# Kernel optimization log

Hardware: AMD Instinct MI355X
Metric: run time of the kernel (lower is better)

Reference implementation:

```python
import jax, jax.numpy as jnp
import numpy as np

N_NODES = 50000
N_EDGES = 600000
D = 128
EPS = 1e-5
AVG_D_LOG = float(np.log(4 + 1))  # avg_d={'log': log(avg_d+1)}, avg_d=4


def setup_inputs() -> dict:
    key = jax.random.key(0)
    ks = jax.random.split(key, 8)
    h = jax.random.normal(ks[0], (N_NODES, D), dtype=jnp.float32)
    # guarantee every node has at least one incoming edge (self-loop)
    edge_dst = jnp.concatenate([
        jnp.arange(N_NODES, dtype=jnp.int64),
        jax.random.randint(ks[1], (N_EDGES - N_NODES,), 0, N_NODES).astype(jnp.int64),
    ])
    edge_src = jax.random.randint(ks[2], (N_EDGES,), 0, N_NODES).astype(jnp.int64)
    def lin(k, fan_in, fan_out):
        lim = 1.0 / np.sqrt(fan_in)
        return jax.random.uniform(k, (fan_in, fan_out), jnp.float32, -lim, lim)
    W_pre = lin(ks[3], 2 * D, D)
    b_pre = jnp.zeros((D,), jnp.float32)
    W_post = lin(ks[4], 12 * D + D, D)  # 4 aggregators * 3 scalers * D + in_dim
    b_post = jnp.zeros((D,), jnp.float32)
    W_mix = lin(ks[5], D, D)
    b_mix = jnp.zeros((D,), jnp.float32)
    return {"h": h, "edge_src": edge_src, "edge_dst": edge_dst,
            "W_pre": W_pre, "b_pre": b_pre, "W_post": W_post,
            "b_post": b_post, "W_mix": W_mix, "b_mix": b_mix}


def reference(h, edge_src, edge_dst, W_pre, b_pre, W_post, b_post, W_mix, b_mix):
    n = h.shape[0]
    # pretrans_edges: cat(src, dst) -> Linear -> ReLU (MLP act) -> ReLU (outer)
    z2 = jnp.concatenate([h[edge_src], h[edge_dst]], axis=1)        # [E, 2D]
    e = jax.nn.relu(z2 @ W_pre + b_pre)                             # [E, D]
    # multi-aggregator segment reduce over destination nodes
    deg = jax.ops.segment_sum(jnp.ones_like(edge_dst, jnp.float32), edge_dst, n)  # [N]
    inv_deg = 1.0 / deg[:, None]
    mean = jax.ops.segment_sum(e, edge_dst, n) * inv_deg
    mean_sq = jax.ops.segment_sum(e * e, edge_dst, n) * inv_deg
    std = jnp.sqrt(jax.nn.relu(mean_sq - mean * mean) + EPS)
    mx = jax.ops.segment_max(e, edge_dst, n)
    mn = jax.ops.segment_min(e, edge_dst, n)
    agg = jnp.concatenate([mean, mx, mn, std], axis=1)              # [N, 4D]
    # scalers: identity, amplification, attenuation
    log_d = jnp.log(deg + 1.0)[:, None]
    scaled = jnp.concatenate([agg, agg * (log_d / AVG_D_LOG), agg * (AVG_D_LOG / log_d)], axis=1)  # [N, 12D]
    # posttrans: cat(h, aggregated) -> Linear -> ReLU
    hp = jax.nn.relu(jnp.concatenate([h, scaled], axis=1) @ W_post + b_post)  # [N, D]
    # mixing network + residual (node_dim == out_dim)
    out = h + jax.nn.leaky_relu(hp @ W_mix + b_mix, negative_slope=0.01)
    return out
```

## Files before the change

### kernel.cpp

```cpp
#include <hip/hip_runtime.h>
#include <hip/hip_bf16.h>

#define N_NODES 50000
#define N_EDGES 600000
#define D 128
#define NB_SCAN 196

constexpr float AVG_D_LOG = 1.6094379124341003f;
constexpr float EPS_V = 1e-5f;

#define PQ_B     0ul
#define AGG_B    25600000ul
#define HBF_B    76800000ul
#define WPRET2_B 89600000ul
#define WPOSTT_B 89665536ul
#define WMIXT_B  90091520ul
#define DEGC_B   90124288ul
#define OFF_B    90324288ul
#define CUR_B    90524352ul
#define SRCS_B   90724352ul
#define BSUM_B   93124352ul

typedef __attribute__((ext_vector_type(8))) short bf16x8;
typedef __attribute__((ext_vector_type(4))) float f32x4;

__device__ __forceinline__ short f2b(float f) {
    unsigned u = __builtin_bit_cast(unsigned, f);
    u += 0x7fffu + ((u >> 16) & 1u);
    return (short)(u >> 16);
}
__device__ __forceinline__ unsigned pk2(float a, float b) {
    return (unsigned)(unsigned short)f2b(a) | ((unsigned)(unsigned short)f2b(b) << 16);
}
__device__ __forceinline__ float blo(unsigned u) { return __uint_as_float(u << 16); }
__device__ __forceinline__ float bhi(unsigned u) { return __uint_as_float(u & 0xffff0000u); }

__device__ __forceinline__ void gld_lds16(const void* g, void* l) {
    __builtin_amdgcn_global_load_lds(
        (const __attribute__((address_space(1))) void*)g,
        (__attribute__((address_space(3))) void*)l, 16, 0, 0);
}

#define WAIT_BAR(N) do {                                              \
    asm volatile("s_waitcnt vmcnt(" #N ")" ::: "memory");             \
    __builtin_amdgcn_sched_barrier(0);                                \
    __builtin_amdgcn_s_barrier();                                     \
    __builtin_amdgcn_sched_barrier(0);                                \
} while (0)
#define BAR_ONLY() do {                                               \
    __builtin_amdgcn_sched_barrier(0);                                \
    __builtin_amdgcn_s_barrier();                                     \
    __builtin_amdgcn_sched_barrier(0);                                \
} while (0)

__global__ __launch_bounds__(256) void prep_kernel(
    const float* __restrict__ h, const float* __restrict__ Wpre,
    const float* __restrict__ Wpost, const float* __restrict__ Wmix,
    short* __restrict__ hbf, short* __restrict__ wpreT2,
    short* __restrict__ wpostT, short* __restrict__ wmixT,
    int* __restrict__ degc, int* __restrict__ cursor)
{
    long i = (long)blockIdx.x * 256 + threadIdx.x;
    if (i < 800000) {
        float4 a = *(const float4*)(h + i * 8);
        float4 b = *(const float4*)(h + i * 8 + 4);
        int4 v;
        v.x = (int)pk2(a.x, a.y); v.y = (int)pk2(a.z, a.w);
        v.z = (int)pk2(b.x, b.y); v.w = (int)pk2(b.z, b.w);
        *(int4*)(hbf + i * 8) = v;
        return;
    }
    i -= 800000;
    if (i < 32768) {
        int n = i >> 7, k = i & 127;
        float v = (n < 128) ? Wpre[k * 128 + n] : Wpre[(k + 128) * 128 + (n - 128)];
        wpreT2[n * 128 + k] = f2b(v);
        return;
    }
    i -= 32768;
    if (i < 212992) { int k = i >> 7, n = i & 127; wpostT[n * 1664 + k] = f2b(Wpost[k * 128 + n]); return; }
    i -= 212992;
    if (i < 16384) { int k = i >> 7, n = i & 127; wmixT[n * 128 + k] = f2b(Wmix[k * 128 + n]); return; }
    i -= 16384;
    if (i < N_NODES) { degc[i] = 0; return; }
    i -= N_NODES;
    if (i < N_NODES) cursor[i] = 0;
}
#define PREP_BLOCKS ((800000 + 32768 + 212992 + 16384 + 2 * N_NODES + 255) / 256)

__global__ __launch_bounds__(256) void hist_kernel(const int* __restrict__ edst, int* __restrict__ degc) {
    int e = blockIdx.x * 256 + threadIdx.x;
    if (e < N_EDGES) atomicAdd(&degc[edst[e]], 1);
}

__global__ __launch_bounds__(256) void scan1_kernel(const int* __restrict__ degc, int* __restrict__ bsum) {
    int n = blockIdx.x * 256 + threadIdx.x;
    int v = (n < N_NODES) ? degc[n] : 0;
#pragma unroll
    for (int o = 32; o > 0; o >>= 1) v += __shfl_down(v, o);
    __shared__ int w4[4];
    if ((threadIdx.x & 63) == 0) w4[threadIdx.x >> 6] = v;
    __syncthreads();
    if (threadIdx.x == 0) bsum[blockIdx.x] = w4[0] + w4[1] + w4[2] + w4[3];
}

__global__ __launch_bounds__(256) void scan2_kernel(int* __restrict__ bsum, int* __restrict__ off) {
    __shared__ int sd[256];
    int tid = threadIdx.x;
    int v = (tid < NB_SCAN) ? bsum[tid] : 0;
    sd[tid] = v;
    __syncthreads();
    for (int o = 1; o < 256; o <<= 1) {
        int t = (tid >= o) ? sd[tid - o] : 0;
        __syncthreads();
        sd[tid] += t;
        __syncthreads();
    }
    if (tid < NB_SCAN) bsum[tid] = sd[tid] - v;
    if (tid == 0) off[N_NODES] = sd[255];
}

__global__ __launch_bounds__(256) void scan3_kernel(const int* __restrict__ degc,
                                                    const int* __restrict__ bsum, int* __restrict__ off) {
    __shared__ int sd[256];
    int tid = threadIdx.x;
    int n = blockIdx.x * 256 + tid;
    int v = (n < N_NODES) ? degc[n] : 0;
    sd[tid] = v;
    __syncthreads();
    for (int o = 1; o < 256; o <<= 1) {
        int t = (tid >= o) ? sd[tid - o] : 0;
        __syncthreads();
        sd[tid] += t;
        __syncthreads();
    }
    if (n < N_NODES) off[n] = sd[tid] - v + bsum[blockIdx.x];
}

__global__ __launch_bounds__(256) void scatter_kernel(const int* __restrict__ esrc, const int* __restrict__ edst,
                                                      const int* __restrict__ off, int* __restrict__ cursor,
                                                      int* __restrict__ srcs) {
    int e = blockIdx.x * 256 + threadIdx.x;
    if (e < N_EDGES) {
        int d = edst[e];
        int p = off[d] + atomicAdd(&cursor[d], 1);
        srcs[p] = esrc[e];
    }
}

__global__ __launch_bounds__(256) void gemm_pq_kernel(
    const short* __restrict__ hbf, const short* __restrict__ wpreT2,
    const float* __restrict__ bpre, short* __restrict__ PQ)
{
    __shared__ __align__(16) short As[128][72];
    __shared__ __align__(16) short Bs[128][72];

    const int tid = threadIdx.x;
    const int cg = blockIdx.x & 1;
    const int bn = (blockIdx.x >> 1) * 128;
    const int lane = tid & 63, wv = tid >> 6;
    const int lm = lane & 15, quad = lane >> 4;

    f32x4 acc[2][8];
#pragma unroll
    for (int a = 0; a < 2; a++)
#pragma unroll
        for (int b = 0; b < 8; b++) acc[a][b] = (f32x4){0.f, 0.f, 0.f, 0.f};

#pragma unroll
    for (int kc = 0; kc < 2; kc++) {
        __syncthreads();
#pragma unroll
        for (int t = 0; t < 4; t++) {
            int q = tid + t * 256;
            int m = q >> 3, seg = q & 7;
            int n = bn + m; if (n >= N_NODES) n = N_NODES - 1;
            *(int4*)&As[m][seg * 8] = *(const int4*)(hbf + (long)n * 128 + kc * 64 + seg * 8);
        }
#pragma unroll
        for (int t = 0; t < 4; t++) {
            int q = tid + t * 256;
            int n = q >> 3, seg = q & 7;
            *(int4*)&Bs[n][seg * 8] = *(const int4*)(wpreT2 + (cg * 128 + n) * 128 + kc * 64 + seg * 8);
        }
        __syncthreads();
#pragma unroll
        for (int ks = 0; ks < 2; ks++) {
            const int ko = ks * 32 + quad * 8;
            bf16x8 a0 = *(const bf16x8*)&As[wv * 32 + lm][ko];
            bf16x8 a1 = *(const bf16x8*)&As[wv * 32 + 16 + lm][ko];
#pragma unroll
            for (int ct = 0; ct < 8; ct++) {
                bf16x8 b = *(const bf16x8*)&Bs[ct * 16 + lm][ko];
                acc[0][ct] = __builtin_amdgcn_mfma_f32_16x16x32_bf16(b, a0, acc[0][ct], 0, 0, 0);
                acc[1][ct] = __builtin_amdgcn_mfma_f32_16x16x32_bf16(b, a1, acc[1][ct], 0, 0, 0);
            }
        }
    }

#pragma unroll
    for (int rt = 0; rt < 2; rt++) {
        int row = wv * 32 + rt * 16 + lm;
        int n = bn + row;
        if (n >= N_NODES) continue;
        short* dst = PQ + (long)n * 256;
#pragma unroll
        for (int ct = 0; ct < 8; ct++) {
            int col = cg * 128 + ct * 16 + quad * 4;
            float v0 = acc[rt][ct][0], v1 = acc[rt][ct][1], v2 = acc[rt][ct][2], v3 = acc[rt][ct][3];
            if (cg) {
                float4 bv = *(const float4*)(bpre + (col - 128));
                v0 += bv.x; v1 += bv.y; v2 += bv.z; v3 += bv.w;
            }
            int2 pkd; pkd.x = (int)pk2(v0, v1); pkd.y = (int)pk2(v2, v3);
            *(int2*)(dst + col) = pkd;
        }
    }
}

__global__ __launch_bounds__(256) void edgestats_kernel(
    const short* __restrict__ PQ, const int* __restrict__ srcs,
    const int* __restrict__ off, short* __restrict__ aggbf)
{
    const int wv = threadIdx.x >> 6, lane = threadIdx.x & 63;
    const int n = blockIdx.x * 4 + wv;
    const unsigned* Pb = (const unsigned*)PQ;

    const int s0 = __builtin_amdgcn_readfirstlane(off[n]);
    const int s1 = __builtin_amdgcn_readfirstlane(off[n + 1]);

    unsigned qu = Pb[(long)n * 128 + 64 + lane];
    const float qa = blo(qu), qb = bhi(qu);

    float sA = 0.f, sB = 0.f, qA = 0.f, qB = 0.f;
    float mxA = -1e30f, mxB = -1e30f, mnA = 1e30f, mnB = 1e30f;

    int p = s0;
    for (; p + 8 <= s1; p += 8) {
        int idx[8];
#pragma unroll
        for (int j = 0; j < 8; j++) idx[j] = srcs[p + j];
        unsigned u[8];
#pragma unroll
        for (int j = 0; j < 8; j++) u[j] = Pb[(long)idx[j] * 128 + lane];
#pragma unroll
        for (int j = 0; j < 8; j++) {
            float a = blo(u[j]) + qa; a = a > 0.f ? a : 0.f;
            float b = bhi(u[j]) + qb; b = b > 0.f ? b : 0.f;
            sA += a; sB += b; qA += a * a; qB += b * b;
            mxA = fmaxf(mxA, a); mxB = fmaxf(mxB, b);
            mnA = fminf(mnA, a); mnB = fminf(mnB, b);
        }
    }
    for (; p < s1; p++) {
        unsigned u = Pb[(long)srcs[p] * 128 + lane];
        float a = blo(u) + qa; a = a > 0.f ? a : 0.f;
        float b = bhi(u) + qb; b = b > 0.f ? b : 0.f;
        sA += a; sB += b; qA += a * a; qB += b * b;
        mxA = fmaxf(mxA, a); mxB = fmaxf(mxB, b);
        mnA = fminf(mnA, a); mnB = fminf(mnB, b);
    }

    float inv = 1.0f / (float)(s1 - s0);
    float mA = sA * inv, mB = sB * inv;
    float vA = qA * inv - mA * mA; vA = vA > 0.f ? vA : 0.f;
    float vB = qB * inv - mB * mB; vB = vB > 0.f ? vB : 0.f;
    float stA = sqrtf(vA + EPS_V), stB = sqrtf(vB + EPS_V);

    unsigned* ag = (unsigned*)(aggbf + (long)n * 512);
    ag[lane]       = pk2(mA, mB);
    ag[64 + lane]  = pk2(mxA, mxB);
    ag[128 + lane] = pk2(mnA, mnB);
    ag[192 + lane] = pk2(stA, stB);
}


__device__ __forceinline__ void stageA_t(short* ldsT, const short* src, int rs, int co,
                                         int bn, int wv, int lane) {
    const int sub = lane >> 3, seg = lane & 7;
    const int sg = (seg ^ sub) * 8;
#pragma unroll
    for (int t = 0; t < 4; t++) {
        int i = wv * 4 + t;
        int row = i * 8 + sub;
        int n = bn + row; if (n >= N_NODES) n = N_NODES - 1;
        gld_lds16(src + (long)n * rs + co + sg, ldsT + i * 512);
    }
}
__device__ __forceinline__ void stageB_t(short* ldsT, const short* src, int rs, int co,
                                         int wv, int lane) {
    const int sub = lane >> 3, seg = lane & 7;
    const int sg = (seg ^ sub) * 8;
#pragma unroll
    for (int t = 0; t < 4; t++) {
        int i = wv * 4 + t;
        int row = i * 8 + sub;
        gld_lds16(src + (long)row * rs + co + sg, ldsT + i * 512);
    }
}

#define MFMA_ITER(AB, BB, ACC)                                                      \
    {                                                                               \
        _Pragma("unroll")                                                           \
        for (int ks = 0; ks < 2; ks++) {                                            \
            const int qx = (((ks * 4 + quad) ^ r7) * 8);                            \
            bf16x8 a0 = *(const bf16x8*)&(AB)[(wv * 32 + lm) * 64 + qx];            \
            bf16x8 a1 = *(const bf16x8*)&(AB)[(wv * 32 + 16 + lm) * 64 + qx];       \
            _Pragma("unroll")                                                       \
            for (int ct = 0; ct < 8; ct++) {                                        \
                bf16x8 b = *(const bf16x8*)&(BB)[(ct * 16 + lm) * 64 + qx];         \
                ACC[0][ct] = __builtin_amdgcn_mfma_f32_16x16x32_bf16(b, a0, ACC[0][ct], 0, 0, 0); \
                ACC[1][ct] = __builtin_amdgcn_mfma_f32_16x16x32_bf16(b, a1, ACC[1][ct], 0, 0, 0); \
            }                                                                       \
        }                                                                           \
    }

__global__ __launch_bounds__(256, 2) void node_kernel(
    const float* __restrict__ h, const short* __restrict__ hbf, const short* __restrict__ aggbf,
    const int* __restrict__ degc, const short* __restrict__ wpostT, const float* __restrict__ bpost,
    const short* __restrict__ wmixT, const float* __restrict__ bmix, float* __restrict__ out)
{
    __shared__ __align__(16) short As[2][8192];
    __shared__ __align__(16) short Bs[2][8192];
    __shared__ float sAmp[128], sAtt[128];

    const int tid = threadIdx.x;
    const int bn = blockIdx.x * 128;
    const int lane = tid & 63, wv = tid >> 6;
    const int lm = lane & 15, quad = lane >> 4;
    const int r7 = lm & 7;

    if (tid < 128) {
        int n = bn + tid; if (n >= N_NODES) n = N_NODES - 1;
        float d = (float)degc[n];
        float ld = logf(d + 1.0f);
        sAmp[tid] = ld * (1.0f / AVG_D_LOG);
        sAtt[tid] = AVG_D_LOG / ld;
    }
    __syncthreads();

    f32x4 accI[2][8], accM[2][8], accT[2][8];
#pragma unroll
    for (int a = 0; a < 2; a++)
#pragma unroll
        for (int b = 0; b < 8; b++) {
            accI[a][b] = (f32x4){0.f, 0.f, 0.f, 0.f};
            accM[a][b] = (f32x4){0.f, 0.f, 0.f, 0.f};
            accT[a][b] = (f32x4){0.f, 0.f, 0.f, 0.f};
        }


    stageA_t(As[0], hbf, 128, 0, bn, wv, lane);
    stageB_t(Bs[0], wpostT, 1664, 0, wv, lane);

    stageA_t(As[1], hbf, 128, 64, bn, wv, lane);
    stageB_t(Bs[1], wpostT, 1664, 64, wv, lane);
    WAIT_BAR(8);
    MFMA_ITER(As[0], Bs[0], accI);
    BAR_ONLY();

    stageB_t(Bs[0], wpostT, 1664, 2 * 64, wv, lane);
    stageA_t(As[0], aggbf, 512, 0, bn, wv, lane);
    WAIT_BAR(8);
    MFMA_ITER(As[1], Bs[1], accI);
    BAR_ONLY();

    int pb = 0;
    for (int j = 0; j < 8; j++) {
        short* Ac = As[j & 1];
        stageB_t(Bs[pb ^ 1], wpostT, 1664, (10 + j) * 64, wv, lane);
        if (j < 7) {
            int jn = j + 1;
            stageA_t(As[jn & 1], aggbf, 512, (jn >> 1) * 128 + (jn & 1) * 64, bn, wv, lane);
            WAIT_BAR(8);
        } else {
            WAIT_BAR(4);
        }
        MFMA_ITER(Ac, Bs[pb], accI);
        BAR_ONLY();

        stageB_t(Bs[pb], wpostT, 1664, (18 + j) * 64, wv, lane);
        if (j < 7) { WAIT_BAR(8); } else { WAIT_BAR(4); }
        MFMA_ITER(Ac, Bs[pb ^ 1], accM);
        BAR_ONLY();

        if (j < 7) stageB_t(Bs[pb ^ 1], wpostT, 1664, (3 + j) * 64, wv, lane);
        else       stageB_t(Bs[pb ^ 1], wmixT, 128, 0, wv, lane);
        WAIT_BAR(4);
        MFMA_ITER(Ac, Bs[pb], accT);
        BAR_ONLY();
        pb ^= 1;
    }

    stageB_t(Bs[1], wmixT, 128, 64, wv, lane);

    const float am0 = sAmp[wv * 32 + lm],      at0 = sAtt[wv * 32 + lm];
    const float am1 = sAmp[wv * 32 + 16 + lm], at1 = sAtt[wv * 32 + 16 + lm];
#pragma unroll
    for (int rt = 0; rt < 2; rt++) {
        const float am = rt ? am1 : am0, at = rt ? at1 : at0;
        const int row = wv * 32 + rt * 16 + lm;
#pragma unroll
        for (int ct = 0; ct < 8; ct++) {
            float4 bv = *(const float4*)(bpost + ct * 16 + quad * 4);
            float v0 = accI[rt][ct][0] + am * accM[rt][ct][0] + at * accT[rt][ct][0] + bv.x;
            float v1 = accI[rt][ct][1] + am * accM[rt][ct][1] + at * accT[rt][ct][1] + bv.y;
            float v2 = accI[rt][ct][2] + am * accM[rt][ct][2] + at * accT[rt][ct][2] + bv.z;
            float v3 = accI[rt][ct][3] + am * accM[rt][ct][3] + at * accT[rt][ct][3] + bv.w;
            v0 = v0 > 0.f ? v0 : 0.f; v1 = v1 > 0.f ? v1 : 0.f;
            v2 = v2 > 0.f ? v2 : 0.f; v3 = v3 > 0.f ? v3 : 0.f;
            int2 pkd; pkd.x = (int)pk2(v0, v1); pkd.y = (int)pk2(v2, v3);
            const int cb = (ct & 3) * 32 + quad * 8;
            const int sb = ((((cb >> 4) ^ r7) << 4) | (cb & 15));
            *(int2*)((char*)As[ct >> 2] + row * 128 + sb) = pkd;
        }
    }
    __syncthreads();

    f32x4 accO[2][8];
#pragma unroll
    for (int a = 0; a < 2; a++)
#pragma unroll
        for (int b = 0; b < 8; b++) accO[a][b] = (f32x4){0.f, 0.f, 0.f, 0.f};
#pragma unroll
    for (int kc = 0; kc < 2; kc++) {
        MFMA_ITER(As[kc], Bs[kc], accO);
    }

#pragma unroll
    for (int rt = 0; rt < 2; rt++) {
        int row = wv * 32 + rt * 16 + lm;
        int n = bn + row;
        if (n >= N_NODES) continue;
#pragma unroll
        for (int ct = 0; ct < 8; ct++) {
            int col = ct * 16 + quad * 4;
            float4 bv = *(const float4*)(bmix + col);
            float4 hv = *(const float4*)(h + (long)n * 128 + col);
            float4 o;
            float v0 = accO[rt][ct][0] + bv.x; v0 = v0 > 0.f ? v0 : 0.01f * v0; o.x = hv.x + v0;
            float v1 = accO[rt][ct][1] + bv.y; v1 = v1 > 0.f ? v1 : 0.01f * v1; o.y = hv.y + v1;
            float v2 = accO[rt][ct][2] + bv.z; v2 = v2 > 0.f ? v2 : 0.01f * v2; o.z = hv.z + v2;
            float v3 = accO[rt][ct][3] + bv.w; v3 = v3 > 0.f ? v3 : 0.01f * v3; o.w = hv.w + v3;
            *(float4*)(out + (long)n * 128 + col) = o;
        }
    }
}

extern "C" void kernel_launch(void* const* d_in, const int* in_sizes, int n_in,
                              void* d_out, int out_size, void* d_ws, size_t ws_size,
                              hipStream_t stream) {
    const float* h     = (const float*)d_in[0];
    const int*   esrc  = (const int*)d_in[1];
    const int*   edst  = (const int*)d_in[2];
    const float* Wpre  = (const float*)d_in[3];
    const float* bpre  = (const float*)d_in[4];
    const float* Wpost = (const float*)d_in[5];
    const float* bpost = (const float*)d_in[6];
    const float* Wmix  = (const float*)d_in[7];
    const float* bmix  = (const float*)d_in[8];
    float* out = (float*)d_out;
    char* ws = (char*)d_ws;

    short* PQ     = (short*)(ws + PQ_B);
    short* aggbf  = (short*)(ws + AGG_B);
    short* hbf    = (short*)(ws + HBF_B);
    short* wpreT2 = (short*)(ws + WPRET2_B);
    short* wpostT = (short*)(ws + WPOSTT_B);
    short* wmixT  = (short*)(ws + WMIXT_B);
    int*   degc   = (int*)(ws + DEGC_B);
    int*   off    = (int*)(ws + OFF_B);
    int*   cursor = (int*)(ws + CUR_B);
    int*   srcs   = (int*)(ws + SRCS_B);
    int*   bsum   = (int*)(ws + BSUM_B);

    prep_kernel<<<PREP_BLOCKS, 256, 0, stream>>>(h, Wpre, Wpost, Wmix, hbf, wpreT2, wpostT, wmixT, degc, cursor);
    hist_kernel<<<(N_EDGES + 255) / 256, 256, 0, stream>>>(edst, degc);
    scan1_kernel<<<NB_SCAN, 256, 0, stream>>>(degc, bsum);
    scan2_kernel<<<1, 256, 0, stream>>>(bsum, off);
    scan3_kernel<<<NB_SCAN, 256, 0, stream>>>(degc, bsum, off);
    scatter_kernel<<<(N_EDGES + 255) / 256, 256, 0, stream>>>(esrc, edst, off, cursor, srcs);
    gemm_pq_kernel<<<((N_NODES + 127) / 128) * 2, 256, 0, stream>>>(hbf, wpreT2, bpre, PQ);
    edgestats_kernel<<<N_NODES / 4, 256, 0, stream>>>(PQ, srcs, off, aggbf);
    node_kernel<<<(N_NODES + 127) / 128, 256, 0, stream>>>(h, hbf, aggbf, degc, wpostT, bpost, wmixT, bmix, out);
}
```

Baseline: 259.9 us.

## Replace three-pass scan with atomic segment allocation; reuse staged MFMA path in PQ GEMM

Replaces the three-kernel exclusive scan with one kernel. Each wavefront computes a local prefix of node degrees and reserves its segment base with an atomicAdd on a global counter, so CSR segments no longer follow node order. The edge-stats kernel now takes segment end from off+degc instead of off[n+1]. The PQ GEMM is rewritten to use the same async LDS staging and MFMA macro as the node kernel, and edgestats gains a 4-edge unrolled tail step. This removes two launches and one serial single-block kernel, at the cost of non-deterministic segment placement and less locality in srcs.

Measured after the change: 254.5 us. 2.1% less time.

```diff
diff --git a/kernel.cpp b/kernel.cpp
--- a/kernel.cpp
+++ b/kernel.cpp
@@ -4,7 +4,6 @@
 #define N_NODES 50000
 #define N_EDGES 600000
 #define D 128
-#define NB_SCAN 196
 
 constexpr float AVG_D_LOG = 1.6094379124341003f;
 constexpr float EPS_V = 1e-5f;
@@ -19,7 +18,7 @@
 #define OFF_B    90324288ul
 #define CUR_B    90524352ul
 #define SRCS_B   90724352ul
-#define BSUM_B   93124352ul
+#define GCNT_B   93124352ul
 
 typedef __attribute__((ext_vector_type(8))) short bf16x8;
 typedef __attribute__((ext_vector_type(4))) float f32x4;
@@ -58,7 +57,7 @@
     const float* __restrict__ Wpost, const float* __restrict__ Wmix,
     short* __restrict__ hbf, short* __restrict__ wpreT2,
     short* __restrict__ wpostT, short* __restrict__ wmixT,
-    int* __restrict__ degc, int* __restrict__ cursor)
+    int* __restrict__ degc, int* __restrict__ cursor, int* __restrict__ gcnt)
 {
     long i = (long)blockIdx.x * 256 + threadIdx.x;
     if (i < 800000) {
@@ -84,57 +83,31 @@
     i -= 16384;
     if (i < N_NODES) { degc[i] = 0; return; }
     i -= N_NODES;
-    if (i < N_NODES) cursor[i] = 0;
-}
-#define PREP_BLOCKS ((800000 + 32768 + 212992 + 16384 + 2 * N_NODES + 255) / 256)
+    if (i < N_NODES) { cursor[i] = 0; return; }
+    i -= N_NODES;
+    if (i == 0) *gcnt = 0;
+}
+#define PREP_BLOCKS ((800000 + 32768 + 212992 + 16384 + 2 * N_NODES + 1 + 255) / 256)
 
 __global__ __launch_bounds__(256) void hist_kernel(const int* __restrict__ edst, int* __restrict__ degc) {
     int e = blockIdx.x * 256 + threadIdx.x;
     if (e < N_EDGES) atomicAdd(&degc[edst[e]], 1);
 }
 
-__global__ __launch_bounds__(256) void scan1_kernel(const int* __restrict__ degc, int* __restrict__ bsum) {
+__global__ __launch_bounds__(256) void alloc_kernel(const int* __restrict__ degc,
+                                                    int* __restrict__ off, int* __restrict__ gcnt) {
     int n = blockIdx.x * 256 + threadIdx.x;
-    int v = (n < N_NODES) ? degc[n] : 0;
-#pragma unroll
-    for (int o = 32; o > 0; o >>= 1) v += __shfl_down(v, o);
-    __shared__ int w4[4];
-    if ((threadIdx.x & 63) == 0) w4[threadIdx.x >> 6] = v;
-    __syncthreads();
-    if (threadIdx.x == 0) bsum[blockIdx.x] = w4[0] + w4[1] + w4[2] + w4[3];
-}
-
-__global__ __launch_bounds__(256) void scan2_kernel(int* __restrict__ bsum, int* __restrict__ off) {
-    __shared__ int sd[256];
-    int tid = threadIdx.x;
-    int v = (tid < NB_SCAN) ? bsum[tid] : 0;
-    sd[tid] = v;
-    __syncthreads();
-    for (int o = 1; o < 256; o <<= 1) {
-        int t = (tid >= o) ? sd[tid - o] : 0;
-        __syncthreads();
-        sd[tid] += t;
-        __syncthreads();
-    }
-    if (tid < NB_SCAN) bsum[tid] = sd[tid] - v;
-    if (tid == 0) off[N_NODES] = sd[255];
-}
-
-__global__ __launch_bounds__(256) void scan3_kernel(const int* __restrict__ degc,
-                                                    const int* __restrict__ bsum, int* __restrict__ off) {
-    __shared__ int sd[256];
-    int tid = threadIdx.x;
-    int n = blockIdx.x * 256 + tid;
-    int v = (n < N_NODES) ? degc[n] : 0;
-    sd[tid] = v;
-    __syncthreads();
-    for (int o = 1; o < 256; o <<= 1) {
-        int t = (tid >= o) ? sd[tid - o] : 0;
-        __syncthreads();
-        sd[tid] += t;
-        __syncthreads();
-    }
-    if (n < N_NODES) off[n] = sd[tid] - v + bsum[blockIdx.x];
+    int d = (n < N_NODES) ? degc[n] : 0;
+    int pre = d;
+#pragma unroll
+    for (int o = 1; o < 64; o <<= 1) {
+        int t = __shfl_up(pre, o);
+        if ((threadIdx.x & 63) >= o) pre += t;
+    }
+    int base = 0;
+    if ((threadIdx.x & 63) == 63) base = atomicAdd(gcnt, pre);
+    base = __shfl(base, 63);
+    if (n < N_NODES) off[n] = base + pre - d;
 }
 
 __global__ __launch_bounds__(256) void scatter_kernel(const int* __restrict__ esrc, const int* __restrict__ edst,
@@ -147,133 +120,6 @@
         srcs[p] = esrc[e];
     }
 }
-
-__global__ __launch_bounds__(256) void gemm_pq_kernel(
-    const short* __restrict__ hbf, const short* __restrict__ wpreT2,
-    const float* __restrict__ bpre, short* __restrict__ PQ)
-{
-    __shared__ __align__(16) short As[128][72];
-    __shared__ __align__(16) short Bs[128][72];
-
-    const int tid = threadIdx.x;
-    const int cg = blockIdx.x & 1;
-    const int bn = (blockIdx.x >> 1) * 128;
-    const int lane = tid & 63, wv = tid >> 6;
-    const int lm = lane & 15, quad = lane >> 4;
-
-    f32x4 acc[2][8];
-#pragma unroll
-    for (int a = 0; a < 2; a++)
-#pragma unroll
-        for (int b = 0; b < 8; b++) acc[a][b] = (f32x4){0.f, 0.f, 0.f, 0.f};
-
-#pragma unroll
-    for (int kc = 0; kc < 2; kc++) {
-        __syncthreads();
-#pragma unroll
-        for (int t = 0; t < 4; t++) {
-            int q = tid + t * 256;
-            int m = q >> 3, seg = q & 7;
-            int n = bn + m; if (n >= N_NODES) n = N_NODES - 1;
-            *(int4*)&As[m][seg * 8] = *(const int4*)(hbf + (long)n * 128 + kc * 64 + seg * 8);
-        }
-#pragma unroll
-        for (int t = 0; t < 4; t++) {
-            int q = tid + t * 256;
-            int n = q >> 3, seg = q & 7;
-            *(int4*)&Bs[n][seg * 8] = *(const int4*)(wpreT2 + (cg * 128 + n) * 128 + kc * 64 + seg * 8);
-        }
-        __syncthreads();
-#pragma unroll
-        for (int ks = 0; ks < 2; ks++) {
-            const int ko = ks * 32 + quad * 8;
-            bf16x8 a0 = *(const bf16x8*)&As[wv * 32 + lm][ko];
-            bf16x8 a1 = *(const bf16x8*)&As[wv * 32 + 16 + lm][ko];
-#pragma unroll
-            for (int ct = 0; ct < 8; ct++) {
-                bf16x8 b = *(const bf16x8*)&Bs[ct * 16 + lm][ko];
-                acc[0][ct] = __builtin_amdgcn_mfma_f32_16x16x32_bf16(b, a0, acc[0][ct], 0, 0, 0);
-                acc[1][ct] = __builtin_amdgcn_mfma_f32_16x16x32_bf16(b, a1, acc[1][ct], 0, 0, 0);
-            }
-        }
-    }
-
-#pragma unroll
-    for (int rt = 0; rt < 2; rt++) {
-        int row = wv * 32 + rt * 16 + lm;
-        int n = bn + row;
-        if (n >= N_NODES) continue;
-        short* dst = PQ + (long)n * 256;
-#pragma unroll
-        for (int ct = 0; ct < 8; ct++) {
-            int col = cg * 128 + ct * 16 + quad * 4;
-            float v0 = acc[rt][ct][0], v1 = acc[rt][ct][1], v2 = acc[rt][ct][2], v3 = acc[rt][ct][3];
-            if (cg) {
-                float4 bv = *(const float4*)(bpre + (col - 128));
-                v0 += bv.x; v1 += bv.y; v2 += bv.z; v3 += bv.w;
-            }
-            int2 pkd; pkd.x = (int)pk2(v0, v1); pkd.y = (int)pk2(v2, v3);
-            *(int2*)(dst + col) = pkd;
-        }
-    }
-}
-
-__global__ __launch_bounds__(256) void edgestats_kernel(
-    const short* __restrict__ PQ, const int* __restrict__ srcs,
-    const int* __restrict__ off, short* __restrict__ aggbf)
-{
-    const int wv = threadIdx.x >> 6, lane = threadIdx.x & 63;
-    const int n = blockIdx.x * 4 + wv;
-    const unsigned* Pb = (const unsigned*)PQ;
-
-    const int s0 = __builtin_amdgcn_readfirstlane(off[n]);
-    const int s1 = __builtin_amdgcn_readfirstlane(off[n + 1]);
-
-    unsigned qu = Pb[(long)n * 128 + 64 + lane];
-    const float qa = blo(qu), qb = bhi(qu);
-
-    float sA = 0.f, sB = 0.f, qA = 0.f, qB = 0.f;
-    float mxA = -1e30f, mxB = -1e30f, mnA = 1e30f, mnB = 1e30f;
-
-    int p = s0;
-    for (; p + 8 <= s1; p += 8) {
-        int idx[8];
-#pragma unroll
-        for (int j = 0; j < 8; j++) idx[j] = srcs[p + j];
-        unsigned u[8];
-#pragma unroll
-        for (int j = 0; j < 8; j++) u[j] = Pb[(long)idx[j] * 128 + lane];
-#pragma unroll
-        for (int j = 0; j < 8; j++) {
-            float a = blo(u[j]) + qa; a = a > 0.f ? a : 0.f;
-            float b = bhi(u[j]) + qb; b = b > 0.f ? b : 0.f;
-            sA += a; sB += b; qA += a * a; qB += b * b;
-            mxA = fmaxf(mxA, a); mxB = fmaxf(mxB, b);
-            mnA = fminf(mnA, a); mnB = fminf(mnB, b);
-        }
-    }
-    for (; p < s1; p++) {
-        unsigned u = Pb[(long)srcs[p] * 128 + lane];
-        float a = blo(u) + qa; a = a > 0.f ? a : 0.f;
-        float b = bhi(u) + qb; b = b > 0.f ? b : 0.f;
-        sA += a; sB += b; qA += a * a; qB += b * b;
-        mxA = fmaxf(mxA, a); mxB = fmaxf(mxB, b);
-        mnA = fminf(mnA, a); mnB = fminf(mnB, b);
-    }
-
-    float inv = 1.0f / (float)(s1 - s0);
-    float mA = sA * inv, mB = sB * inv;
-    float vA = qA * inv - mA * mA; vA = vA > 0.f ? vA : 0.f;
-    float vB = qB * inv - mB * mB; vB = vB > 0.f ? vB : 0.f;
-    float stA = sqrtf(vA + EPS_V), stB = sqrtf(vB + EPS_V);
-
-    unsigned* ag = (unsigned*)(aggbf + (long)n * 512);
-    ag[lane]       = pk2(mA, mB);
-    ag[64 + lane]  = pk2(mxA, mxB);
-    ag[128 + lane] = pk2(mnA, mnB);
-    ag[192 + lane] = pk2(stA, stB);
-}
-
 
 __device__ __forceinline__ void stageA_t(short* ldsT, const short* src, int rs, int co,
                                          int bn, int wv, int lane) {
@@ -315,6 +161,129 @@
         }                                                                           \
     }
 
+__global__ __launch_bounds__(256, 2) void gemm_pq_kernel(
+    const short* __restrict__ hbf, const short* __restrict__ wpreT2,
+    const float* __restrict__ bpre, short* __restrict__ PQ)
+{
+    __shared__ __align__(16) short As[2][8192];
+    __shared__ __align__(16) short Bs[2][8192];
+
+    const int tid = threadIdx.x;
+    const int cg = blockIdx.x & 1;
+    const int bn = (blockIdx.x >> 1) * 128;
+    const int lane = tid & 63, wv = tid >> 6;
+    const int lm = lane & 15, quad = lane >> 4;
+    const int r7 = lm & 7;
+    const short* Bsrc = wpreT2 + cg * 128 * 128;
+
+    f32x4 acc[2][8];
+#pragma unroll
+    for (int a = 0; a < 2; a++)
+#pragma unroll
+        for (int b = 0; b < 8; b++) acc[a][b] = (f32x4){0.f, 0.f, 0.f, 0.f};
+
+    stageA_t(As[0], hbf, 128, 0, bn, wv, lane);
+    stageB_t(Bs[0], Bsrc, 128, 0, wv, lane);
+    stageA_t(As[1], hbf, 128, 64, bn, wv, lane);
+    stageB_t(Bs[1], Bsrc, 128, 64, wv, lane);
+    WAIT_BAR(8);
+    MFMA_ITER(As[0], Bs[0], acc);
+    WAIT_BAR(0);
+    MFMA_ITER(As[1], Bs[1], acc);
+
+#pragma unroll
+    for (int rt = 0; rt < 2; rt++) {
+        int row = wv * 32 + rt * 16 + lm;
+        int n = bn + row;
+        if (n >= N_NODES) continue;
+        short* dst = PQ + (long)n * 256;
+#pragma unroll
+        for (int ct = 0; ct < 8; ct++) {
+            int col = cg * 128 + ct * 16 + quad * 4;
+            float v0 = acc[rt][ct][0], v1 = acc[rt][ct][1], v2 = acc[rt][ct][2], v3 = acc[rt][ct][3];
+            if (cg) {
+                float4 bv = *(const float4*)(bpre + (col - 128));
+                v0 += bv.x; v1 += bv.y; v2 += bv.z; v3 += bv.w;
+            }
+            int2 pkd; pkd.x = (int)pk2(v0, v1); pkd.y = (int)pk2(v2, v3);
+            *(int2*)(dst + col) = pkd;
+        }
+    }
+}
+
+__global__ __launch_bounds__(256) void edgestats_kernel(
+    const short* __restrict__ PQ, const int* __restrict__ srcs,
+    const int* __restrict__ off, const int* __restrict__ degc, short* __restrict__ aggbf)
+{
+    const int wv = threadIdx.x >> 6, lane = threadIdx.x & 63;
+    const int n = blockIdx.x * 4 + wv;
+    const unsigned* Pb = (const unsigned*)PQ;
+
+    const int s0 = __builtin_amdgcn_readfirstlane(off[n]);
+    const int s1 = s0 + __builtin_amdgcn_readfirstlane(degc[n]);
+
+    unsigned qu = Pb[(long)n * 128 + 64 + lane];
+    const float qa = blo(qu), qb = bhi(qu);
+
+    float sA = 0.f, sB = 0.f, qA = 0.f, qB = 0.f;
+    float mxA = -1e30f, mxB = -1e30f, mnA = 1e30f, mnB = 1e30f;
+
+    int p = s0;
+    for (; p + 8 <= s1; p += 8) {
+        int idx[8];
+#pragma unroll
+        for (int j = 0; j < 8; j++) idx[j] = srcs[p + j];
+        unsigned u[8];
+#pragma unroll
+        for (int j = 0; j < 8; j++) u[j] = Pb[(long)idx[j] * 128 + lane];
+#pragma unroll
+        for (int j = 0; j < 8; j++) {
+            float a = blo(u[j]) + qa; a = a > 0.f ? a : 0.f;
+            float b = bhi(u[j]) + qb; b = b > 0.f ? b : 0.f;
+            sA += a; sB += b; qA += a * a; qB += b * b;
+            mxA = fmaxf(mxA, a); mxB = fmaxf(mxB, b);
+            mnA = fminf(mnA, a); mnB = fminf(mnB, b);
+        }
+    }
+    if (p + 4 <= s1) {
+        int idx[4];
+#pragma unroll
+        for (int j = 0; j < 4; j++) idx[j] = srcs[p + j];
+        unsigned u[4];
+#pragma unroll
+        for (int j = 0; j < 4; j++) u[j] = Pb[(long)idx[j] * 128 + lane];
+#pragma unroll
+        for (int j = 0; j < 4; j++) {
+            float a = blo(u[j]) + qa; a = a > 0.f ? a : 0.f;
+            float b = bhi(u[j]) + qb; b = b > 0.f ? b : 0.f;
+            sA += a; sB += b; qA += a * a; qB += b * b;
+            mxA = fmaxf(mxA, a); mxB = fmaxf(mxB, b);
+            mnA = fminf(mnA, a); mnB = fminf(mnB, b);
+        }
+        p += 4;
+    }
+    for (; p < s1; p++) {
+        unsigned u = Pb[(long)srcs[p] * 128 + lane];
+        float a = blo(u) + qa; a = a > 0.f ? a : 0.f;
+        float b = bhi(u) + qb; b = b > 0.f ? b : 0.f;
+        sA += a; sB += b; qA += a * a; qB += b * b;
+        mxA = fmaxf(mxA, a); mxB = fmaxf(mxB, b);
+        mnA = fminf(mnA, a); mnB = fminf(mnB, b);
+    }
+
+    float inv = 1.0f / (float)(s1 - s0);
+    float mA = sA * inv, mB = sB * inv;
+    float vA = qA * inv - mA * mA; vA = vA > 0.f ? vA : 0.f;
+    float vB = qB * inv - mB * mB; vB = vB > 0.f ? vB : 0.f;
+    float stA = sqrtf(vA + EPS_V), stB = sqrtf(vB + EPS_V);
+
+    unsigned* ag = (unsigned*)(aggbf + (long)n * 512);
+    ag[lane]       = pk2(mA, mB);
+    ag[64 + lane]  = pk2(mxA, mxB);
+    ag[128 + lane] = pk2(mnA, mnB);
+    ag[192 + lane] = pk2(stA, stB);
+}
+
 __global__ __launch_bounds__(256, 2) void node_kernel(
     const float* __restrict__ h, const short* __restrict__ hbf, const short* __restrict__ aggbf,
     const int* __restrict__ degc, const short* __restrict__ wpostT, const float* __restrict__ bpost,
@@ -367,7 +336,7 @@
 
     int pb = 0;
     for (int j = 0; j < 8; j++) {
-        short* Ac = As[j & 1];
+        const short* Ac = As[j & 1];
         stageB_t(Bs[pb ^ 1], wpostT, 1664, (10 + j) * 64, wv, lane);
         if (j < 7) {
             int jn = j + 1;
@@ -472,15 +441,13 @@
     int*   off    = (int*)(ws + OFF_B);
     int*   cursor = (int*)(ws + CUR_B);
     int*   srcs   = (int*)(ws + SRCS_B);
-    int*   bsum   = (int*)(ws + BSUM_B);
-
-    prep_kernel<<<PREP_BLOCKS, 256, 0, stream>>>(h, Wpre, Wpost, Wmix, hbf, wpreT2, wpostT, wmixT, degc, cursor);
+    int*   gcnt   = (int*)(ws + GCNT_B);
+
+    prep_kernel<<<PREP_BLOCKS, 256, 0, stream>>>(h, Wpre, Wpost, Wmix, hbf, wpreT2, wpostT, wmixT, degc, cursor, gcnt);
     hist_kernel<<<(N_EDGES + 255) / 256, 256, 0, stream>>>(edst, degc);
-    scan1_kernel<<<NB_SCAN, 256, 0, stream>>>(degc, bsum);
-    scan2_kernel<<<1, 256, 0, stream>>>(bsum, off);
-    scan3_kernel<<<NB_SCAN, 256, 0, stream>>>(degc, bsum, off);
+    alloc_kernel<<<(N_NODES + 255) / 256, 256, 0, stream>>>(degc, off, gcnt);
     scatter_kernel<<<(N_EDGES + 255) / 256, 256, 0, stream>>>(esrc, edst, off, cursor, srcs);
     gemm_pq_kernel<<<((N_NODES + 127) / 128) * 2, 256, 0, stream>>>(hbf, wpreT2, bpre, PQ);
-    edgestats_kernel<<<N_NODES / 4, 256, 0, stream>>>(PQ, srcs, off, aggbf);
+    edgestats_kernel<<<N_NODES / 4, 256, 0, stream>>>(PQ, srcs, off, degc, aggbf);
     node_kernel<<<(N_NODES + 127) / 128, 256, 0, stream>>>(h, hbf, aggbf, degc, wpostT, bpost, wmixT, bmix, out);
 }
```
